# Kernel tuning notes

Measured on AMD Instinct MI355X. Metric: run time of the kernel, lower is better.

Reference implementation:

```python
import jax, jax.numpy as jnp
import numpy as np
from jax import lax

N, CIN, H, W = 16, 3, 512, 512
BH = BW = 16  # block size (h, w); bstride == bsize so blocks tile the image
EPS = 1e-5


def setup_inputs() -> dict:
    key = jax.random.key(0)
    ks = jax.random.split(key, 32)
    def nrm(k, shape, s=0.05):
        return jax.random.normal(k, shape, jnp.float32) * s
    def bnp(k, ch):
        # rows: gamma, beta, running_mean, running_var (var kept > 0)
        u = jax.random.uniform(k, (4, ch), jnp.float32)
        return u.at[3].add(0.1)
    feat = (H // 4) * (W // 4) * 8
    return {
        "x": jax.random.normal(ks[0], (N, CIN, H, W), jnp.float32),
        "mask": jax.random.uniform(ks[1], (N, 1, H, W), jnp.float32),
        "s1_cw": nrm(ks[2], (16, CIN, 1, 1)), "s1_cb": nrm(ks[3], (16,)), "s1_bn0": bnp(ks[4], 16),
        "s1_d1w": nrm(ks[5], (32, 16, 1, 1)), "s1_d1b": nrm(ks[6], (32,)), "s1_bn1": bnp(ks[7], 32),
        "s1_d2w": nrm(ks[8], (32, 32, 3, 3)), "s1_d2b": nrm(ks[9], (32,)), "s1_bn2": bnp(ks[10], 32),
        "s1_d3w": nrm(ks[11], (16, 32, 1, 1)), "s1_d3b": nrm(ks[12], (16,)), "s1_bn3": bnp(ks[13], 16),
        "s2_cw": nrm(ks[14], (8, 16, 1, 1)), "s2_cb": nrm(ks[15], (8,)), "s2_bn0": bnp(ks[16], 8),
        "s2_d1w": nrm(ks[17], (16, 8, 1, 1)), "s2_d1b": nrm(ks[18], (16,)), "s2_bn1": bnp(ks[19], 16),
        "s2_d2w": nrm(ks[20], (16, 16, 3, 3)), "s2_d2b": nrm(ks[21], (16,)), "s2_bn2": bnp(ks[22], 16),
        "s2_d3w": nrm(ks[23], (8, 16, 1, 1)), "s2_d3b": nrm(ks[24], (8,)), "s2_bn3": bnp(ks[25], 8),
        "fc_w": nrm(ks[26], (10, feat), 0.01), "fc_b": nrm(ks[27], (10,)),
    }


def conv(x, w, b, p):
    y = lax.conv_general_dilated(x, w, (1, 1), [(p, p), (p, p)],
                                 dimension_numbers=("NCHW", "OIHW", "NCHW"))
    return y + b[None, :, None, None]


def bnorm(x, p):
    g, bt, m, v = p[0], p[1], p[2], p[3]
    scale = g * lax.rsqrt(v + EPS)
    return scale[None, :, None, None] * (x - m[None, :, None, None]) + bt[None, :, None, None]


def to_blocks(x):
    # [N,C,H,W] -> [N*nby*nbx, C, BH, BW]
    n, c, hh, ww = x.shape
    nby, nbx = hh // BH, ww // BW
    b = x.reshape(n, c, nby, BH, nbx, BW).transpose(0, 2, 4, 1, 3, 5)
    return b.reshape(n * nby * nbx, c, BH, BW), (n, nby, nbx)


def from_blocks(b, meta, c):
    n, nby, nbx = meta
    x = b.reshape(n, nby, nbx, c, BH, BW).transpose(0, 3, 1, 4, 2, 5)
    return x.reshape(n, c, nby * BH, nbx * BW)


def maxpool2(x):
    return lax.reduce_window(x, -jnp.inf, lax.max, (1, 1, 2, 2), (1, 1, 2, 2), "VALID")


def sparse_conv_block(x, mask, cw, cb, bn0, d1w, d1b, bn1, d2w, d2b, bn2, d3w, d3b, bn3):
    # reduce_mask: block is active if its mean mask value exceeds threshold
    mblocks, _ = to_blocks(mask)
    active = mblocks.mean(axis=(1, 2, 3)) > 0.5  # [N*nblocks]
    # channel path (applies to every pixel)
    xc = bnorm(jax.nn.relu(conv(x, cw, cb, 0)), bn0)
    # gather -> dense bottleneck convs per block (3x3 padded within each block) -> scatter
    blocks, meta = to_blocks(xc)
    g = bnorm(jax.nn.relu(conv(blocks, d1w, d1b, 0)), bn1)
    g = bnorm(jax.nn.relu(conv(g, d2w, d2b, 1)), bn2)
    g = bnorm(jax.nn.relu(conv(g, d3w, d3b, 0)), bn3)
    out = jnp.where(active[:, None, None, None], g, blocks)
    return from_blocks(out, meta, xc.shape[1])


def reference(x, mask, s1_cw, s1_cb, s1_bn0, s1_d1w, s1_d1b, s1_bn1, s1_d2w, s1_d2b, s1_bn2,
              s1_d3w, s1_d3b, s1_bn3, s2_cw, s2_cb, s2_bn0, s2_d1w, s2_d1b, s2_bn1,
              s2_d2w, s2_d2b, s2_bn2, s2_d3w, s2_d3b, s2_bn3, fc_w, fc_b):
    x1 = sparse_conv_block(x, mask, s1_cw, s1_cb, s1_bn0, s1_d1w, s1_d1b, s1_bn1,
                           s1_d2w, s1_d2b, s1_bn2, s1_d3w, s1_d3b, s1_bn3)
    x1 = maxpool2(x1)
    mask2 = maxpool2(mask)
    x2 = sparse_conv_block(x1, mask2, s2_cw, s2_cb, s2_bn0, s2_d1w, s2_d1b, s2_bn1,
                           s2_d2w, s2_d2b, s2_bn2, s2_d3w, s2_d3b, s2_bn3)
    x2 = maxpool2(x2)
    flat = x2.reshape(x2.shape[0], -1)  # [N, (H/4)*(W/4)*8]
    logits = flat @ fc_w.T + fc_b
    return jax.nn.softmax(logits, axis=-1)
```

## Files before the change

### kernel.cpp

```cpp
#include <hip/hip_runtime.h>
#include <math.h>


typedef __attribute__((ext_vector_type(8))) short bf16x8;
typedef __attribute__((ext_vector_type(4))) float f32x4;

#define X1P_OFF 0
#define X2_OFF  16777216
#define LG_OFF  18874368
#define MS_OFF  18874624
#define P_OFF   18878720

enum : int {
  WT_S1C  = 0,
  WT_S2C  = 48,
  SC_S1BN0 = 176,
  SC_S1BN1 = 208,
  SC_S1BN2 = 272,
  SC_S1BN3 = 336,
  SC_S2BN0 = 368,
  SC_S2BN1 = 384,
  SC_S2BN2 = 416,
  SC_S2BN3 = 448,
  PH_F     = 464
};
enum : int {
  H_S1D2 = 0,
  H_S1D3 = 9216,
  H_S2D2 = 9728,
  H_S2D3 = 12288,
  H_S1D1 = 12544,
  H_S2D1 = 13568,
  PH_END = 14080
};

__device__ __forceinline__ float relu_f(float v) { return v > 0.f ? v : 0.f; }

__device__ __forceinline__ unsigned short f2bf(float f) {
  unsigned int u = __float_as_uint(f);
  unsigned int r = (u + 0x7fffu + ((u >> 16) & 1u)) >> 16;
  return (unsigned short)r;
}

__device__ __forceinline__ unsigned int pk2(float lo, float hi) {
  unsigned int r;
  asm("v_cvt_pk_bf16_f32 %0, %1, %2" : "=v"(r) : "v"(lo), "v"(hi));
  return r;
}

__device__ __forceinline__ void prep_bn(const float* __restrict__ p, int C,
                                        float* __restrict__ dst, int t) {
  for (int i = t; i < C; i += 256) {
    float g = p[i], b = p[C + i], m = p[2 * C + i], v = p[3 * C + i];
    float s = g / sqrtf(v + 1e-5f);
    dst[i] = s;
    dst[C + i] = b - s * m;
  }
}

__global__ __launch_bounds__(256) void prep_kernel(
    const float* __restrict__ s1_cw, const float* __restrict__ s1_d1w,
    const float* __restrict__ s1_d2w, const float* __restrict__ s1_d3w,
    const float* __restrict__ s2_cw, const float* __restrict__ s2_d1w,
    const float* __restrict__ s2_d2w, const float* __restrict__ s2_d3w,
    const float* __restrict__ s1_bn0, const float* __restrict__ s1_bn1,
    const float* __restrict__ s1_bn2, const float* __restrict__ s1_bn3,
    const float* __restrict__ s2_bn0, const float* __restrict__ s2_bn1,
    const float* __restrict__ s2_bn2, const float* __restrict__ s2_bn3,
    float* __restrict__ P, float* __restrict__ lg, float* __restrict__ ms) {
  const int t = threadIdx.x;
  unsigned short* PH = (unsigned short*)(P + PH_F);
  for (int i = t; i < 48;  i += 256) { int co = i / 3,  ci = i % 3;  P[WT_S1C + ci * 16 + co] = s1_cw[i]; }
  for (int i = t; i < 128; i += 256) { int co = i / 16, ci = i % 16; P[WT_S2C + ci * 8  + co] = s2_cw[i]; }
  for (int i = t; i < 9216; i += 256) {
    int tap = i >> 10, o = (i >> 5) & 31, ci = i & 31;
    PH[H_S1D2 + i] = f2bf(s1_d2w[o * 288 + ci * 9 + tap]);
  }
  for (int i = t; i < 512; i += 256) PH[H_S1D3 + i] = f2bf(s1_d3w[i]);
  for (int i = t; i < 2560; i += 256) {
    int p = i >> 9, o = (i >> 5) & 15, k = i & 31;
    int tp = 2 * p + (k >> 4);
    PH[H_S2D2 + i] = (tp < 9) ? f2bf(s2_d2w[o * 144 + (k & 15) * 9 + tp]) : 0;
  }
  for (int i = t; i < 256; i += 256) {
    int nn = i >> 4, k = i & 15;
    PH[H_S2D3 + i] = (nn < 8) ? f2bf(s2_d3w[nn * 16 + k]) : 0;
  }
  for (int i = t; i < 1024; i += 256) {
    int o = i >> 5, k = i & 31;
    PH[H_S1D1 + i] = (k < 16) ? f2bf(s1_d1w[o * 16 + k]) : 0;
  }
  for (int i = t; i < 512; i += 256) {
    int o = i >> 5, k = i & 31;
    PH[H_S2D1 + i] = (k < 8) ? f2bf(s2_d1w[o * 8 + k]) : 0;
  }
  prep_bn(s1_bn0, 16, P + SC_S1BN0, t);
  prep_bn(s1_bn1, 32, P + SC_S1BN1, t);
  prep_bn(s1_bn2, 32, P + SC_S1BN2, t);
  prep_bn(s1_bn3, 16, P + SC_S1BN3, t);
  prep_bn(s2_bn0, 8,  P + SC_S2BN0, t);
  prep_bn(s2_bn1, 16, P + SC_S2BN1, t);
  prep_bn(s2_bn2, 16, P + SC_S2BN2, t);
  prep_bn(s2_bn3, 8,  P + SC_S2BN3, t);
  if (t < 160) lg[t] = 0.f;
  for (int i = t; i < 4096; i += 256) ms[i] = 0.f;
}

__global__ __launch_bounds__(256, 4) void stage1_kernel(
    const float* __restrict__ x, const float* __restrict__ mask,
    const float* __restrict__ cbv, const float* __restrict__ d1b,
    const float* __restrict__ d2b, const float* __restrict__ d3b,
    const float* __restrict__ P, float* __restrict__ x1p,
    float* __restrict__ msum) {
  __shared__ __align__(16) unsigned char ldsb[25920];
  __shared__ float red_s[4], red_v[4];

  const int t = threadIdx.x;
  const int ty = t >> 4, tx = t & 15;
  const int b = blockIdx.x;
  const int n = b >> 10;
  const int by = (b >> 5) & 31, bx = b & 31;
  const int gy = by * 16 + ty, gx = bx * 16 + tx;

  {
    const float m = mask[(size_t)(n * 512 + gy) * 512 + gx];
    float v = fmaxf(m, __shfl_xor(m, 1, 64));
    v = fmaxf(v, __shfl_xor(v, 16, 64));
    float s = m;
    #pragma unroll
    for (int off = 32; off > 0; off >>= 1) {
      s += __shfl_down(s, off, 64);
      v += __shfl_down(v, off, 64);
    }
    if ((t & 63) == 0) { red_s[t >> 6] = s; red_v[t >> 6] = v; }
  }
  __syncthreads();

  float xin[3];
  #pragma unroll
  for (int c = 0; c < 3; ++c)
    xin[c] = x[(size_t)((n * 3 + c) * 512 + gy) * 512 + gx];

  const float* wc = P + WT_S1C;
  const float* sc0 = P + SC_S1BN0;
  float xc[16];
  {
    float a[16];
    #pragma unroll
    for (int o = 0; o < 16; ++o) a[o] = cbv[o];
    #pragma unroll
    for (int c = 0; c < 3; ++c) {
      const float v = xin[c];
      #pragma unroll
      for (int o = 0; o < 16; ++o) a[o] = fmaf(wc[c * 16 + o], v, a[o]);
    }
    #pragma unroll
    for (int o = 0; o < 16; ++o) xc[o] = fmaf(sc0[o], relu_f(a[o]), sc0[16 + o]);
  }

  const bool active = (red_s[0] + red_s[1] + red_s[2] + red_s[3]) > 128.0f;
  if (t == 0)
    atomicAdd(&msum[n * 256 + (by >> 1) * 16 + (bx >> 1)],
              (red_v[0] + red_v[1] + red_v[2] + red_v[3]) * 0.25f);

  float* const poolf = (float*)(ldsb + 20480);

  if (active) {
    const int w = t >> 6, lane = t & 63;
    const int lr = lane & 15, cb = lane >> 4;
    const unsigned short* PH = (const unsigned short*)(P + PH_F);

    if (t < 68) {
      int row, col;
      if (t < 18)      { row = 0;      col = t;      }
      else if (t < 36) { row = 17;     col = t - 18; }
      else if (t < 52) { row = t - 35; col = 0;      }
      else             { row = t - 51; col = 17;     }
      uint4* z = (uint4*)(ldsb + (row * 18 + col) * 80);
      const uint4 z4 = make_uint4(0u, 0u, 0u, 0u);
      z[0] = z4; z[1] = z4; z[2] = z4; z[3] = z4;
    }
    {
      unsigned int pk[8];
      #pragma unroll
      for (int i = 0; i < 8; ++i) pk[i] = pk2(xc[2 * i], xc[2 * i + 1]);
      uint4* dst = (uint4*)(ldsb + ((ty + 1) * 18 + (tx + 1)) * 80);
      dst[0] = make_uint4(pk[0], pk[1], pk[2], pk[3]);
      dst[1] = make_uint4(pk[4], pk[5], pk[6], pk[7]);
    }

    {
      bf16x8 w1f[2];
      #pragma unroll
      for (int ct = 0; ct < 2; ++ct)
        w1f[ct] = *(const bf16x8*)(PH + H_S1D1 + (ct * 16 + lr) * 32 + cb * 8);
      f32x4 acc1[2][4];
      #pragma unroll
      for (int ct = 0; ct < 2; ++ct) {
        const float4 bb = *(const float4*)(d1b + ct * 16 + cb * 4);
        #pragma unroll
        for (int nt = 0; nt < 4; ++nt) {
          acc1[ct][nt][0] = bb.x; acc1[ct][nt][1] = bb.y;
          acc1[ct][nt][2] = bb.z; acc1[ct][nt][3] = bb.w;
        }
      }
      #pragma unroll
      for (int nt = 0; nt < 4; ++nt) {
        bf16x8 xcf;
        if (cb < 2) xcf = *(const bf16x8*)(ldsb + ((w * 4 + nt + 1) * 18 + lr + 1) * 80 + cb * 16);
        else        xcf = (bf16x8)(short)0;
        #pragma unroll
        for (int ct = 0; ct < 2; ++ct)
          acc1[ct][nt] = __builtin_amdgcn_mfma_f32_16x16x32_bf16(w1f[ct], xcf, acc1[ct][nt], 0, 0, 0);
      }
      #pragma unroll
      for (int ct = 0; ct < 2; ++ct) {
        const float4 s1s = *(const float4*)(P + SC_S1BN1 + ct * 16 + cb * 4);
        const float4 s1h = *(const float4*)(P + SC_S1BN1 + 32 + ct * 16 + cb * 4);
        #pragma unroll
        for (int nt = 0; nt < 4; ++nt) {
          const unsigned base = ((w * 4 + nt + 1) * 18 + lr + 1) * 80 + (ct * 16 + cb * 4) * 2;
          *(unsigned int*)(ldsb + base) =
              pk2(fmaf(s1s.x, relu_f(acc1[ct][nt][0]), s1h.x),
                  fmaf(s1s.y, relu_f(acc1[ct][nt][1]), s1h.y));
          *(unsigned int*)(ldsb + base + 4) =
              pk2(fmaf(s1s.z, relu_f(acc1[ct][nt][2]), s1h.z),
                  fmaf(s1s.w, relu_f(acc1[ct][nt][3]), s1h.w));
        }
      }
    }
    __syncthreads();

    const int ct3 = w & 1, ph = w >> 1;
    f32x4 acc2[8];
    {
      const float4 bb = *(const float4*)(d2b + ct3 * 16 + cb * 4);
      #pragma unroll
      for (int q = 0; q < 8; ++q) {
        acc2[q][0] = bb.x; acc2[q][1] = bb.y; acc2[q][2] = bb.z; acc2[q][3] = bb.w;
      }
    }
    #pragma clang loop unroll(disable)
    for (int dy = 0; dy < 3; ++dy) {
      bf16x8 bwr[3];
      #pragma unroll
      for (int dx = 0; dx < 3; ++dx)
        bwr[dx] = *(const bf16x8*)(PH + H_S1D2 + ((dy * 3 + dx) * 32 + ct3 * 16 + lr) * 32 + cb * 8);
      const int rb = (ph * 8 + dy) * 18 + lr;
      #pragma unroll
      for (int dx = 0; dx < 3; ++dx)
        #pragma unroll
        for (int q = 0; q < 8; ++q) {
          const bf16x8 af = *(const bf16x8*)(ldsb + (rb + q * 18 + dx) * 80 + cb * 16);
          acc2[q] = __builtin_amdgcn_mfma_f32_16x16x32_bf16(bwr[dx], af, acc2[q], 0, 0, 0);
        }
    }
    __syncthreads();

    {
      const float4 s2s = *(const float4*)(P + SC_S1BN2 + ct3 * 16 + cb * 4);
      const float4 s2h = *(const float4*)(P + SC_S1BN2 + 32 + ct3 * 16 + cb * 4);
      #pragma unroll
      for (int q = 0; q < 8; ++q) {
        const int pix = (ph * 8 + q) * 16 + lr;
        const unsigned base = pix * 80 + (ct3 * 16 + cb * 4) * 2;
        *(unsigned int*)(ldsb + base) =
            pk2(fmaf(s2s.x, relu_f(acc2[q][0]), s2h.x),
                fmaf(s2s.y, relu_f(acc2[q][1]), s2h.y));
        *(unsigned int*)(ldsb + base + 4) =
            pk2(fmaf(s2s.z, relu_f(acc2[q][2]), s2h.z),
                fmaf(s2s.w, relu_f(acc2[q][3]), s2h.w));
      }
    }
    __syncthreads();

    const bf16x8 b3 = *(const bf16x8*)(PH + H_S1D3 + lr * 32 + cb * 8);
    const float bias3v = d3b[lr];
    const float sc3v = P[SC_S1BN3 + lr], sh3v = P[SC_S1BN3 + 16 + lr];
    f32x4 acc3[4];
    #pragma unroll
    for (int mt = 0; mt < 4; ++mt) {
      acc3[mt][0] = bias3v; acc3[mt][1] = bias3v; acc3[mt][2] = bias3v; acc3[mt][3] = bias3v;
      const bf16x8 a3 = *(const bf16x8*)(ldsb + (w * 64 + mt * 16 + lr) * 80 + cb * 16);
      acc3[mt] = __builtin_amdgcn_mfma_f32_16x16x32_bf16(a3, b3, acc3[mt], 0, 0, 0);
    }
    #pragma unroll
    for (int mtp = 0; mtp < 2; ++mtp) {
      float o0[4], o1[4];
      #pragma unroll
      for (int r = 0; r < 4; ++r) {
        o0[r] = fmaf(sc3v, relu_f(acc3[2 * mtp][r]), sh3v);
        o1[r] = fmaf(sc3v, relu_f(acc3[2 * mtp + 1][r]), sh3v);
      }
      #pragma unroll
      for (int rp = 0; rp < 2; ++rp) {
        const float m = fmaxf(fmaxf(o0[2 * rp], o0[2 * rp + 1]),
                              fmaxf(o1[2 * rp], o1[2 * rp + 1]));
        poolf[lr * 68 + (w * 2 + mtp) * 8 + cb * 2 + rp] = m;
      }
    }
  } else {
    float* ldsf = (float*)ldsb;
    {
      float* pw = &ldsf[t * 20];
      #pragma unroll
      for (int c = 0; c < 16; ++c) pw[c] = xc[c];
    }
    __syncthreads();
    {
      const int pp = t & 63, cg = t >> 6;
      const int py = pp >> 3, px = pp & 7;
      const float* r0 = &ldsf[((2 * py) * 16 + 2 * px) * 20 + cg * 4];
      const float* r2 = &ldsf[((2 * py + 1) * 16 + 2 * px) * 20 + cg * 4];
      const float4 v0 = *(const float4*)(r0);
      const float4 v1 = *(const float4*)(r0 + 20);
      const float4 v2 = *(const float4*)(r2);
      const float4 v3 = *(const float4*)(r2 + 20);
      poolf[(cg * 4 + 0) * 68 + py * 8 + px] = fmaxf(fmaxf(v0.x, v1.x), fmaxf(v2.x, v3.x));
      poolf[(cg * 4 + 1) * 68 + py * 8 + px] = fmaxf(fmaxf(v0.y, v1.y), fmaxf(v2.y, v3.y));
      poolf[(cg * 4 + 2) * 68 + py * 8 + px] = fmaxf(fmaxf(v0.z, v1.z), fmaxf(v2.z, v3.z));
      poolf[(cg * 4 + 3) * 68 + py * 8 + px] = fmaxf(fmaxf(v0.w, v1.w), fmaxf(v2.w, v3.w));
    }
  }

  __syncthreads();
  {
    const int ch = t >> 4, idx = t & 15, yy = idx >> 1, h = idx & 1;
    const uint4 v = *(const uint4*)(poolf + ch * 68 + yy * 8 + h * 4);
    const size_t ob = ((((size_t)n * 16 + (by >> 1)) * 16 + (bx >> 1)) * 16 + ch) * 256
                      + (size_t)((by & 1) * 8 + yy) * 16 + (bx & 1) * 8 + h * 4;
    *(uint4*)(x1p + ob) = v;
  }
}

__global__ __launch_bounds__(256, 5) void stage2_kernel(
    const float* __restrict__ msum,
    const float* __restrict__ cbv, const float* __restrict__ d1b,
    const float* __restrict__ d2b, const float* __restrict__ d3b,
    const float* __restrict__ P, const float* __restrict__ x1p,
    float* __restrict__ x2) {
  __shared__ __align__(16) unsigned char ldsb2[15552];

  const int t = threadIdx.x;
  const int ty = t >> 4, tx = t & 15;
  const int b = blockIdx.x;
  const int n = b >> 8;
  const int BY = (b >> 4) & 15, BX = b & 15;

  const bool active = msum[b] > 128.0f;

  const float* xb = x1p + (size_t)b * 4096 + ty * 16 + tx;
  float xin[16];
  #pragma unroll
  for (int c = 0; c < 16; ++c) xin[c] = xb[c * 256];

  const float* wc = P + WT_S2C;
  const float* sc0 = P + SC_S2BN0;
  float xc[8];
  {
    float a[8];
    #pragma unroll
    for (int o = 0; o < 8; ++o) a[o] = cbv[o];
    #pragma unroll
    for (int c = 0; c < 16; ++c) {
      const float v = xin[c];
      #pragma unroll
      for (int o = 0; o < 8; ++o) a[o] = fmaf(wc[c * 8 + o], v, a[o]);
    }
    #pragma unroll
    for (int o = 0; o < 8; ++o) xc[o] = fmaf(sc0[o], relu_f(a[o]), sc0[8 + o]);
  }

  float* const poolf = (float*)(ldsb2 + 12288);

  if (active) {
    const int w = t >> 6, lane = t & 63;
    const int lr = lane & 15, cb = lane >> 4;
    const unsigned short* PH = (const unsigned short*)(P + PH_F);

    if (t < 68) {
      int row, col;
      if (t < 18)      { row = 0;      col = t;      }
      else if (t < 36) { row = 17;     col = t - 18; }
      else if (t < 52) { row = t - 35; col = 0;      }
      else             { row = t - 51; col = 17;     }
      uint4* z = (uint4*)(ldsb2 + (row * 18 + col) * 48);
      const uint4 z4 = make_uint4(0u, 0u, 0u, 0u);
      z[0] = z4; z[1] = z4;
    }
    {
      unsigned int pk[4];
      #pragma unroll
      for (int i = 0; i < 4; ++i) pk[i] = pk2(xc[2 * i], xc[2 * i + 1]);
      *(uint4*)(ldsb2 + ((ty + 1) * 18 + (tx + 1)) * 48) = make_uint4(pk[0], pk[1], pk[2], pk[3]);
    }

    {
      const bf16x8 w1f = *(const bf16x8*)(PH + H_S2D1 + lr * 32 + cb * 8);
      f32x4 acc1[4];
      {
        const float4 bb = *(const float4*)(d1b + cb * 4);
        #pragma unroll
        for (int nt = 0; nt < 4; ++nt) {
          acc1[nt][0] = bb.x; acc1[nt][1] = bb.y; acc1[nt][2] = bb.z; acc1[nt][3] = bb.w;
        }
      }
      #pragma unroll
      for (int nt = 0; nt < 4; ++nt) {
        bf16x8 xcf;
        if (cb == 0) xcf = *(const bf16x8*)(ldsb2 + ((w * 4 + nt + 1) * 18 + lr + 1) * 48);
        else         xcf = (bf16x8)(short)0;
        acc1[nt] = __builtin_amdgcn_mfma_f32_16x16x32_bf16(w1f, xcf, acc1[nt], 0, 0, 0);
      }
      {
        const float4 s1s = *(const float4*)(P + SC_S2BN1 + cb * 4);
        const float4 s1h = *(const float4*)(P + SC_S2BN1 + 16 + cb * 4);
        #pragma unroll
        for (int nt = 0; nt < 4; ++nt) {
          const unsigned base = ((w * 4 + nt + 1) * 18 + lr + 1) * 48 + cb * 8;
          *(unsigned int*)(ldsb2 + base) =
              pk2(fmaf(s1s.x, relu_f(acc1[nt][0]), s1h.x),
                  fmaf(s1s.y, relu_f(acc1[nt][1]), s1h.y));
          *(unsigned int*)(ldsb2 + base + 4) =
              pk2(fmaf(s1s.z, relu_f(acc1[nt][2]), s1h.z),
                  fmaf(s1s.w, relu_f(acc1[nt][3]), s1h.w));
        }
      }
    }
    __syncthreads();

    f32x4 acc2[4];
    {
      const float4 bb = *(const float4*)(d2b + cb * 4);
      #pragma unroll
      for (int nt = 0; nt < 4; ++nt) {
        acc2[nt][0] = bb.x; acc2[nt][1] = bb.y; acc2[nt][2] = bb.z; acc2[nt][3] = bb.w;
      }
    }
    #pragma clang loop unroll(disable)
    for (int p = 0; p < 5; ++p) {
      const bf16x8 bwp = *(const bf16x8*)(PH + H_S2D2 + (p * 16 + lr) * 32 + cb * 8);
      const int tp = (p < 4) ? (2 * p + (cb >> 1)) : 8;
      const int dy = (tp >= 6) ? 2 : ((tp >= 3) ? 1 : 0);
      const int dx = tp - dy * 3;
      #pragma unroll
      for (int nt = 0; nt < 4; ++nt) {
        const bf16x8 af = *(const bf16x8*)(ldsb2 + ((w * 4 + nt + dy) * 18 + lr + dx) * 48 + (cb & 1) * 16);
        acc2[nt] = __builtin_amdgcn_mfma_f32_16x16x32_bf16(bwp, af, acc2[nt], 0, 0, 0);
      }
    }
    __syncthreads();

    {
      const float4 s2s = *(const float4*)(P + SC_S2BN2 + cb * 4);
      const float4 s2h = *(const float4*)(P + SC_S2BN2 + 16 + cb * 4);
      #pragma unroll
      for (int nt = 0; nt < 4; ++nt) {
        const int pix = w * 64 + nt * 16 + lr;
        const unsigned base = pix * 48 + cb * 8;
        *(unsigned int*)(ldsb2 + base) =
            pk2(fmaf(s2s.x, relu_f(acc2[nt][0]), s2h.x),
                fmaf(s2s.y, relu_f(acc2[nt][1]), s2h.y));
        *(unsigned int*)(ldsb2 + base + 4) =
            pk2(fmaf(s2s.z, relu_f(acc2[nt][2]), s2h.z),
                fmaf(s2s.w, relu_f(acc2[nt][3]), s2h.w));
      }
    }
    __syncthreads();

    bf16x8 b3;
    if (cb < 2) b3 = *(const bf16x8*)(PH + H_S2D3 + lr * 16 + cb * 8);
    else        b3 = (bf16x8)(short)0;
    const float bias3v = (lr < 8) ? d3b[lr] : 0.f;
    const float sc3v = (lr < 8) ? P[SC_S2BN3 + lr] : 0.f;
    const float sh3v = (lr < 8) ? P[SC_S2BN3 + 8 + lr] : 0.f;
    f32x4 acc3[4];
    #pragma unroll
    for (int mt = 0; mt < 4; ++mt) {
      acc3[mt][0] = bias3v; acc3[mt][1] = bias3v; acc3[mt][2] = bias3v; acc3[mt][3] = bias3v;
      bf16x8 a3;
      if (cb < 2) a3 = *(const bf16x8*)(ldsb2 + (w * 64 + mt * 16 + lr) * 48 + cb * 16);
      else        a3 = (bf16x8)(short)0;
      acc3[mt] = __builtin_amdgcn_mfma_f32_16x16x32_bf16(a3, b3, acc3[mt], 0, 0, 0);
    }
    if (lr < 8) {
      #pragma unroll
      for (int mtp = 0; mtp < 2; ++mtp) {
        float o0[4], o1[4];
        #pragma unroll
        for (int r = 0; r < 4; ++r) {
          o0[r] = fmaf(sc3v, relu_f(acc3[2 * mtp][r]), sh3v);
          o1[r] = fmaf(sc3v, relu_f(acc3[2 * mtp + 1][r]), sh3v);
        }
        #pragma unroll
        for (int rp = 0; rp < 2; ++rp) {
          const float m = fmaxf(fmaxf(o0[2 * rp], o0[2 * rp + 1]),
                                fmaxf(o1[2 * rp], o1[2 * rp + 1]));
          poolf[lr * 68 + (w * 2 + mtp) * 8 + cb * 2 + rp] = m;
        }
      }
    }
  } else {
    float* ldsf = (float*)ldsb2;
    {
      float* pw = &ldsf[t * 12];
      #pragma unroll
      for (int c = 0; c < 8; ++c) pw[c] = xc[c];
    }
    __syncthreads();
    if (t < 128) {
      const int pp = t & 63, cg = t >> 6;
      const int py = pp >> 3, px = pp & 7;
      const float* r0 = &ldsf[((2 * py) * 16 + 2 * px) * 12 + cg * 4];
      const float* r2 = &ldsf[((2 * py + 1) * 16 + 2 * px) * 12 + cg * 4];
      const float4 v0 = *(const float4*)(r0);
      const float4 v1 = *(const float4*)(r0 + 12);
      const float4 v2 = *(const float4*)(r2);
      const float4 v3 = *(const float4*)(r2 + 12);
      poolf[(cg * 4 + 0) * 68 + py * 8 + px] = fmaxf(fmaxf(v0.x, v1.x), fmaxf(v2.x, v3.x));
      poolf[(cg * 4 + 1) * 68 + py * 8 + px] = fmaxf(fmaxf(v0.y, v1.y), fmaxf(v2.y, v3.y));
      poolf[(cg * 4 + 2) * 68 + py * 8 + px] = fmaxf(fmaxf(v0.z, v1.z), fmaxf(v2.z, v3.z));
      poolf[(cg * 4 + 3) * 68 + py * 8 + px] = fmaxf(fmaxf(v0.w, v1.w), fmaxf(v2.w, v3.w));
    }
  }

  __syncthreads();
  if (t < 128) {
    const int ch = t >> 4, idx = t & 15, yy = idx >> 1, h = idx & 1;
    const uint4 v = *(const uint4*)(poolf + ch * 68 + yy * 8 + h * 4);
    const size_t ob = ((size_t)(n * 8 + ch) * 128 + (BY * 8 + yy)) * 128 + BX * 8 + h * 4;
    *(uint4*)(x2 + ob) = v;
  }
}

__global__ __launch_bounds__(256) void fc_kernel(const float* __restrict__ x2,
                                                 const float* __restrict__ fcw,
                                                 const float* __restrict__ fcb,
                                                 float* __restrict__ logits) {
  __shared__ float red[4];
  const int wg = blockIdx.x, t = threadIdx.x;
  const int sp = wg & 7, k = (wg >> 3) % 10, n = wg / 80;
  const float4* xa = (const float4*)(x2 + (size_t)n * 131072) + sp * 4096;
  const float4* wa = (const float4*)(fcw + (size_t)k * 131072) + sp * 4096;
  float s = 0.f;
  #pragma unroll 4
  for (int i = t; i < 4096; i += 256) {
    const float4 a = xa[i], b = wa[i];
    s = fmaf(a.x, b.x, fmaf(a.y, b.y, fmaf(a.z, b.z, fmaf(a.w, b.w, s))));
  }
  #pragma unroll
  for (int off = 32; off > 0; off >>= 1) s += __shfl_down(s, off, 64);
  if ((t & 63) == 0) red[t >> 6] = s;
  __syncthreads();
  if (t == 0) {
    float tot = red[0] + red[1] + red[2] + red[3];
    if (sp == 0) tot += fcb[k];
    atomicAdd(&logits[n * 10 + k], tot);
  }
}

__global__ void softmax_kernel(const float* __restrict__ logits, float* __restrict__ out) {
  const int t = threadIdx.x;
  if (t < 16) {
    float l[10], mx = -1e30f;
    #pragma unroll
    for (int k = 0; k < 10; ++k) { l[k] = logits[t * 10 + k]; mx = fmaxf(mx, l[k]); }
    float sum = 0.f;
    #pragma unroll
    for (int k = 0; k < 10; ++k) { l[k] = expf(l[k] - mx); sum += l[k]; }
    const float inv = 1.f / sum;
    #pragma unroll
    for (int k = 0; k < 10; ++k) out[t * 10 + k] = l[k] * inv;
  }
}

extern "C" void kernel_launch(void* const* d_in, const int* in_sizes, int n_in,
                              void* d_out, int out_size, void* d_ws, size_t ws_size,
                              hipStream_t stream) {
  const float* x      = (const float*)d_in[0];
  const float* mask   = (const float*)d_in[1];
  const float* s1_cw  = (const float*)d_in[2];
  const float* s1_cb  = (const float*)d_in[3];
  const float* s1_bn0 = (const float*)d_in[4];
  const float* s1_d1w = (const float*)d_in[5];
  const float* s1_d1b = (const float*)d_in[6];
  const float* s1_bn1 = (const float*)d_in[7];
  const float* s1_d2w = (const float*)d_in[8];
  const float* s1_d2b = (const float*)d_in[9];
  const float* s1_bn2 = (const float*)d_in[10];
  const float* s1_d3w = (const float*)d_in[11];
  const float* s1_d3b = (const float*)d_in[12];
  const float* s1_bn3 = (const float*)d_in[13];
  const float* s2_cw  = (const float*)d_in[14];
  const float* s2_cb  = (const float*)d_in[15];
  const float* s2_bn0 = (const float*)d_in[16];
  const float* s2_d1w = (const float*)d_in[17];
  const float* s2_d1b = (const float*)d_in[18];
  const float* s2_bn1 = (const float*)d_in[19];
  const float* s2_d2w = (const float*)d_in[20];
  const float* s2_d2b = (const float*)d_in[21];
  const float* s2_bn2 = (const float*)d_in[22];
  const float* s2_d3w = (const float*)d_in[23];
  const float* s2_d3b = (const float*)d_in[24];
  const float* s2_bn3 = (const float*)d_in[25];
  const float* fc_w   = (const float*)d_in[26];
  const float* fc_b   = (const float*)d_in[27];

  float* ws  = (float*)d_ws;
  float* x1p = ws + X1P_OFF;
  float* x2  = ws + X2_OFF;
  float* lg  = ws + LG_OFF;
  float* ms  = ws + MS_OFF;
  float* P   = ws + P_OFF;

  prep_kernel<<<1, 256, 0, stream>>>(s1_cw, s1_d1w, s1_d2w, s1_d3w,
                                     s2_cw, s2_d1w, s2_d2w, s2_d3w,
                                     s1_bn0, s1_bn1, s1_bn2, s1_bn3,
                                     s2_bn0, s2_bn1, s2_bn2, s2_bn3, P, lg, ms);
  stage1_kernel<<<16 * 32 * 32, 256, 0, stream>>>(x, mask, s1_cb, s1_d1b, s1_d2b, s1_d3b, P, x1p, ms);
  stage2_kernel<<<16 * 16 * 16, 256, 0, stream>>>(ms, s2_cb, s2_d1b, s2_d2b, s2_d3b, P, x1p, x2);
  fc_kernel<<<1280, 256, 0, stream>>>(x2, fc_w, fc_b, lg);
  softmax_kernel<<<1, 64, 0, stream>>>(lg, (float*)d_out);
}
```

Before: 284.7 us.

## Use 32x32x16 MFMA for stage1 3x3 conv, widen LDS stores, parallelize prep

Rewrites the stage-1 3x3 conv to use 32x32x16 bf16 MFMA tiles covering all 32 output channels and 64 pixels per wave, replacing the 16x16x32 layout. The aim is more data reuse per LDS fragment load and fewer MFMA issues. Paired bf16 LDS stores become single 64-bit stores. The prep kernel now spreads its weight and BN setup over 32 blocks instead of one. The new MFMA layout changes register pressure and the LDS access pattern, which could cause bank conflicts.

Result: faster. 276.4 us (-2.9%).

```diff
diff --git a/kernel.cpp b/kernel.cpp
--- a/kernel.cpp
+++ b/kernel.cpp
@@ -4,6 +4,7 @@
 
 typedef __attribute__((ext_vector_type(8))) short bf16x8;
 typedef __attribute__((ext_vector_type(4))) float f32x4;
+typedef __attribute__((ext_vector_type(16))) float f32x16;
 
 #define X1P_OFF 0
 #define X2_OFF  16777216
@@ -49,8 +50,8 @@
 }
 
 __device__ __forceinline__ void prep_bn(const float* __restrict__ p, int C,
-                                        float* __restrict__ dst, int t) {
-  for (int i = t; i < C; i += 256) {
+                                        float* __restrict__ dst, int gid) {
+  for (int i = gid; i < C; i += 8192) {
     float g = p[i], b = p[C + i], m = p[2 * C + i], v = p[3 * C + i];
     float s = g / sqrtf(v + 1e-5f);
     dst[i] = s;
@@ -68,42 +69,42 @@
     const float* __restrict__ s2_bn0, const float* __restrict__ s2_bn1,
     const float* __restrict__ s2_bn2, const float* __restrict__ s2_bn3,
     float* __restrict__ P, float* __restrict__ lg, float* __restrict__ ms) {
-  const int t = threadIdx.x;
+  const int gid = blockIdx.x * 256 + threadIdx.x;
   unsigned short* PH = (unsigned short*)(P + PH_F);
-  for (int i = t; i < 48;  i += 256) { int co = i / 3,  ci = i % 3;  P[WT_S1C + ci * 16 + co] = s1_cw[i]; }
-  for (int i = t; i < 128; i += 256) { int co = i / 16, ci = i % 16; P[WT_S2C + ci * 8  + co] = s2_cw[i]; }
-  for (int i = t; i < 9216; i += 256) {
+  for (int i = gid; i < 48;  i += 8192) { int co = i / 3,  ci = i % 3;  P[WT_S1C + ci * 16 + co] = s1_cw[i]; }
+  for (int i = gid; i < 128; i += 8192) { int co = i / 16, ci = i % 16; P[WT_S2C + ci * 8  + co] = s2_cw[i]; }
+  for (int i = gid; i < 9216; i += 8192) {
     int tap = i >> 10, o = (i >> 5) & 31, ci = i & 31;
     PH[H_S1D2 + i] = f2bf(s1_d2w[o * 288 + ci * 9 + tap]);
   }
-  for (int i = t; i < 512; i += 256) PH[H_S1D3 + i] = f2bf(s1_d3w[i]);
-  for (int i = t; i < 2560; i += 256) {
+  for (int i = gid; i < 512; i += 8192) PH[H_S1D3 + i] = f2bf(s1_d3w[i]);
+  for (int i = gid; i < 2560; i += 8192) {
     int p = i >> 9, o = (i >> 5) & 15, k = i & 31;
     int tp = 2 * p + (k >> 4);
     PH[H_S2D2 + i] = (tp < 9) ? f2bf(s2_d2w[o * 144 + (k & 15) * 9 + tp]) : 0;
   }
-  for (int i = t; i < 256; i += 256) {
+  for (int i = gid; i < 256; i += 8192) {
     int nn = i >> 4, k = i & 15;
     PH[H_S2D3 + i] = (nn < 8) ? f2bf(s2_d3w[nn * 16 + k]) : 0;
   }
-  for (int i = t; i < 1024; i += 256) {
+  for (int i = gid; i < 1024; i += 8192) {
     int o = i >> 5, k = i & 31;
     PH[H_S1D1 + i] = (k < 16) ? f2bf(s1_d1w[o * 16 + k]) : 0;
   }
-  for (int i = t; i < 512; i += 256) {
+  for (int i = gid; i < 512; i += 8192) {
     int o = i >> 5, k = i & 31;
     PH[H_S2D1 + i] = (k < 8) ? f2bf(s2_d1w[o * 8 + k]) : 0;
   }
-  prep_bn(s1_bn0, 16, P + SC_S1BN0, t);
-  prep_bn(s1_bn1, 32, P + SC_S1BN1, t);
-  prep_bn(s1_bn2, 32, P + SC_S1BN2, t);
-  prep_bn(s1_bn3, 16, P + SC_S1BN3, t);
-  prep_bn(s2_bn0, 8,  P + SC_S2BN0, t);
-  prep_bn(s2_bn1, 16, P + SC_S2BN1, t);
-  prep_bn(s2_bn2, 16, P + SC_S2BN2, t);
-  prep_bn(s2_bn3, 8,  P + SC_S2BN3, t);
-  if (t < 160) lg[t] = 0.f;
-  for (int i = t; i < 4096; i += 256) ms[i] = 0.f;
+  prep_bn(s1_bn0, 16, P + SC_S1BN0, gid);
+  prep_bn(s1_bn1, 32, P + SC_S1BN1, gid);
+  prep_bn(s1_bn2, 32, P + SC_S1BN2, gid);
+  prep_bn(s1_bn3, 16, P + SC_S1BN3, gid);
+  prep_bn(s2_bn0, 8,  P + SC_S2BN0, gid);
+  prep_bn(s2_bn1, 16, P + SC_S2BN1, gid);
+  prep_bn(s2_bn2, 16, P + SC_S2BN2, gid);
+  prep_bn(s2_bn3, 8,  P + SC_S2BN3, gid);
+  if (gid < 160) lg[gid] = 0.f;
+  for (int i = gid; i < 4096; i += 8192) ms[i] = 0.f;
 }
 
 __global__ __launch_bounds__(256, 4) void stage1_kernel(
@@ -220,56 +221,67 @@
         #pragma unroll
         for (int nt = 0; nt < 4; ++nt) {
           const unsigned base = ((w * 4 + nt + 1) * 18 + lr + 1) * 80 + (ct * 16 + cb * 4) * 2;
-          *(unsigned int*)(ldsb + base) =
-              pk2(fmaf(s1s.x, relu_f(acc1[ct][nt][0]), s1h.x),
-                  fmaf(s1s.y, relu_f(acc1[ct][nt][1]), s1h.y));
-          *(unsigned int*)(ldsb + base + 4) =
-              pk2(fmaf(s1s.z, relu_f(acc1[ct][nt][2]), s1h.z),
-                  fmaf(s1s.w, relu_f(acc1[ct][nt][3]), s1h.w));
+          uint2 wv;
+          wv.x = pk2(fmaf(s1s.x, relu_f(acc1[ct][nt][0]), s1h.x),
+                     fmaf(s1s.y, relu_f(acc1[ct][nt][1]), s1h.y));
+          wv.y = pk2(fmaf(s1s.z, relu_f(acc1[ct][nt][2]), s1h.z),
+                     fmaf(s1s.w, relu_f(acc1[ct][nt][3]), s1h.w));
+          *(uint2*)(ldsb + base) = wv;
         }
       }
     }
     __syncthreads();
 
-    const int ct3 = w & 1, ph = w >> 1;
-    f32x4 acc2[8];
-    {
-      const float4 bb = *(const float4*)(d2b + ct3 * 16 + cb * 4);
-      #pragma unroll
-      for (int q = 0; q < 8; ++q) {
-        acc2[q][0] = bb.x; acc2[q][1] = bb.y; acc2[q][2] = bb.z; acc2[q][3] = bb.w;
+    const int lane31 = lane & 31;
+    const int prow = lane31 >> 4, pcol = lane & 15, kh = lane >> 5;
+    f32x16 acc2[2];
+    {
+      float4 bb2[4];
+      #pragma unroll
+      for (int g = 0; g < 4; ++g) bb2[g] = *(const float4*)(d2b + 8 * g + 4 * kh);
+      #pragma unroll
+      for (int mti = 0; mti < 2; ++mti) {
+        #pragma unroll
+        for (int g = 0; g < 4; ++g) {
+          acc2[mti][4 * g + 0] = bb2[g].x; acc2[mti][4 * g + 1] = bb2[g].y;
+          acc2[mti][4 * g + 2] = bb2[g].z; acc2[mti][4 * g + 3] = bb2[g].w;
+        }
       }
     }
     #pragma clang loop unroll(disable)
     for (int dy = 0; dy < 3; ++dy) {
-      bf16x8 bwr[3];
+      bf16x8 aw[3][2];
       #pragma unroll
       for (int dx = 0; dx < 3; ++dx)
-        bwr[dx] = *(const bf16x8*)(PH + H_S1D2 + ((dy * 3 + dx) * 32 + ct3 * 16 + lr) * 32 + cb * 8);
-      const int rb = (ph * 8 + dy) * 18 + lr;
+        #pragma unroll
+        for (int ch = 0; ch < 2; ++ch)
+          aw[dx][ch] = *(const bf16x8*)(PH + H_S1D2 + ((dy * 3 + dx) * 32 + lane31) * 32 + ch * 16 + kh * 8);
+      const unsigned char* bp = ldsb + ((w * 4 + prow + dy) * 18 + pcol) * 80 + kh * 16;
       #pragma unroll
       for (int dx = 0; dx < 3; ++dx)
         #pragma unroll
-        for (int q = 0; q < 8; ++q) {
-          const bf16x8 af = *(const bf16x8*)(ldsb + (rb + q * 18 + dx) * 80 + cb * 16);
-          acc2[q] = __builtin_amdgcn_mfma_f32_16x16x32_bf16(bwr[dx], af, acc2[q], 0, 0, 0);
-        }
-    }
-    __syncthreads();
-
-    {
-      const float4 s2s = *(const float4*)(P + SC_S1BN2 + ct3 * 16 + cb * 4);
-      const float4 s2h = *(const float4*)(P + SC_S1BN2 + 32 + ct3 * 16 + cb * 4);
-      #pragma unroll
-      for (int q = 0; q < 8; ++q) {
-        const int pix = (ph * 8 + q) * 16 + lr;
-        const unsigned base = pix * 80 + (ct3 * 16 + cb * 4) * 2;
-        *(unsigned int*)(ldsb + base) =
-            pk2(fmaf(s2s.x, relu_f(acc2[q][0]), s2h.x),
-                fmaf(s2s.y, relu_f(acc2[q][1]), s2h.y));
-        *(unsigned int*)(ldsb + base + 4) =
-            pk2(fmaf(s2s.z, relu_f(acc2[q][2]), s2h.z),
-                fmaf(s2s.w, relu_f(acc2[q][3]), s2h.w));
+        for (int mti = 0; mti < 2; ++mti)
+          #pragma unroll
+          for (int ch = 0; ch < 2; ++ch) {
+            const bf16x8 bf = *(const bf16x8*)(bp + mti * 2880 + dx * 80 + ch * 32);
+            acc2[mti] = __builtin_amdgcn_mfma_f32_32x32x16_bf16(aw[dx][ch], bf, acc2[mti], 0, 0, 0);
+          }
+    }
+    __syncthreads();
+
+    #pragma unroll
+    for (int mti = 0; mti < 2; ++mti) {
+      const int pix = (w * 2 + mti) * 32 + lane31;
+      #pragma unroll
+      for (int g = 0; g < 4; ++g) {
+        const float4 ss = *(const float4*)(P + SC_S1BN2 + 8 * g + 4 * kh);
+        const float4 sh = *(const float4*)(P + SC_S1BN2 + 32 + 8 * g + 4 * kh);
+        uint2 wv;
+        wv.x = pk2(fmaf(ss.x, relu_f(acc2[mti][4 * g + 0]), sh.x),
+                   fmaf(ss.y, relu_f(acc2[mti][4 * g + 1]), sh.y));
+        wv.y = pk2(fmaf(ss.z, relu_f(acc2[mti][4 * g + 2]), sh.z),
+                   fmaf(ss.w, relu_f(acc2[mti][4 * g + 3]), sh.w));
+        *(uint2*)(ldsb + pix * 80 + (8 * g + 4 * kh) * 2) = wv;
       }
     }
     __syncthreads();
@@ -418,12 +430,12 @@
         #pragma unroll
         for (int nt = 0; nt < 4; ++nt) {
           const unsigned base = ((w * 4 + nt + 1) * 18 + lr + 1) * 48 + cb * 8;
-          *(unsigned int*)(ldsb2 + base) =
-              pk2(fmaf(s1s.x, relu_f(acc1[nt][0]), s1h.x),
-                  fmaf(s1s.y, relu_f(acc1[nt][1]), s1h.y));
-          *(unsigned int*)(ldsb2 + base + 4) =
-              pk2(fmaf(s1s.z, relu_f(acc1[nt][2]), s1h.z),
-                  fmaf(s1s.w, relu_f(acc1[nt][3]), s1h.w));
+          uint2 wv;
+          wv.x = pk2(fmaf(s1s.x, relu_f(acc1[nt][0]), s1h.x),
+                     fmaf(s1s.y, relu_f(acc1[nt][1]), s1h.y));
+          wv.y = pk2(fmaf(s1s.z, relu_f(acc1[nt][2]), s1h.z),
+                     fmaf(s1s.w, relu_f(acc1[nt][3]), s1h.w));
+          *(uint2*)(ldsb2 + base) = wv;
         }
       }
     }
@@ -458,12 +470,12 @@
       for (int nt = 0; nt < 4; ++nt) {
         const int pix = w * 64 + nt * 16 + lr;
         const unsigned base = pix * 48 + cb * 8;
-        *(unsigned int*)(ldsb2 + base) =
-            pk2(fmaf(s2s.x, relu_f(acc2[nt][0]), s2h.x),
-                fmaf(s2s.y, relu_f(acc2[nt][1]), s2h.y));
-        *(unsigned int*)(ldsb2 + base + 4) =
-            pk2(fmaf(s2s.z, relu_f(acc2[nt][2]), s2h.z),
-                fmaf(s2s.w, relu_f(acc2[nt][3]), s2h.w));
+        uint2 wv;
+        wv.x = pk2(fmaf(s2s.x, relu_f(acc2[nt][0]), s2h.x),
+                   fmaf(s2s.y, relu_f(acc2[nt][1]), s2h.y));
+        wv.y = pk2(fmaf(s2s.z, relu_f(acc2[nt][2]), s2h.z),
+                   fmaf(s2s.w, relu_f(acc2[nt][3]), s2h.w));
+        *(uint2*)(ldsb2 + base) = wv;
       }
     }
     __syncthreads();
@@ -613,10 +625,10 @@
   float* ms  = ws + MS_OFF;
   float* P   = ws + P_OFF;
 
-  prep_kernel<<<1, 256, 0, stream>>>(s1_cw, s1_d1w, s1_d2w, s1_d3w,
-                                     s2_cw, s2_d1w, s2_d2w, s2_d3w,
-                                     s1_bn0, s1_bn1, s1_bn2, s1_bn3,
-                                     s2_bn0, s2_bn1, s2_bn2, s2_bn3, P, lg, ms);
+  prep_kernel<<<32, 256, 0, stream>>>(s1_cw, s1_d1w, s1_d2w, s1_d3w,
+                                      s2_cw, s2_d1w, s2_d2w, s2_d3w,
+                                      s1_bn0, s1_bn1, s1_bn2, s1_bn3,
+                                      s2_bn0, s2_bn1, s2_bn2, s2_bn3, P, lg, ms);
   stage1_kernel<<<16 * 32 * 32, 256, 0, stream>>>(x, mask, s1_cb, s1_d1b, s1_d2b, s1_d3b, P, x1p, ms);
   stage2_kernel<<<16 * 16 * 16, 256, 0, stream>>>(ms, s2_cb, s2_d1b, s2_d2b, s2_d3b, P, x1p, x2);
   fc_kernel<<<1280, 256, 0, stream>>>(x2, fc_w, fc_b, lg);
```
